# Kernel tuning notes

Measured on AMD Instinct MI355X. Metric: run time of the kernel, lower is better.

Reference implementation:

```python
import jax, jax.numpy as jnp
from jax import lax
import numpy as np

B, S, IN = 8, 4096, 64
D, H, K = 512, 8, 3
TCN_CH = [256, 256, 512]
HD = D // H


def setup_inputs() -> dict:
    key = jax.random.key(0)
    ks = iter(jax.random.split(key, 64))
    def nrm(shape, s=0.02):
        return jax.random.normal(next(ks), shape, jnp.float32) * s
    inp = {"x": jax.random.normal(next(ks), (B, S, IN), jnp.float32)}
    inp["W_in"] = nrm((IN, D)); inp["b_in"] = jnp.zeros((D,), jnp.float32)
    chans = [D] + TCN_CH
    for i in range(3):
        cin, cout = chans[i], chans[i + 1]
        inp[f"c1w{i}"] = nrm((cout, cin, K), 0.01); inp[f"c1b{i}"] = jnp.zeros((cout,), jnp.float32)
        inp[f"c2w{i}"] = nrm((cout, cout, K), 0.01); inp[f"c2b{i}"] = jnp.zeros((cout,), jnp.float32)
        if cin != cout:  # downsample 1x1 conv (blocks 0 and 2)
            inp[f"dsw{i}"] = nrm((cout, cin, 1), 0.01); inp[f"dsb{i}"] = jnp.zeros((cout,), jnp.float32)
    inp["W_tcn"] = nrm((TCN_CH[-1], D)); inp["b_tcn"] = jnp.zeros((D,), jnp.float32)
    NL = 2  # attention layers, stacked on leading axis
    for n in ["Wq", "Wk", "Wv", "Wo"]:
        inp[n] = nrm((NL, D, D))
    for n in ["bq", "bk", "bv", "bo", "ln_b"]:
        inp[n] = jnp.zeros((NL, D), jnp.float32)
    inp["ln_g"] = jnp.ones((NL, D), jnp.float32)
    inp["W_out"] = nrm((D, 1)); inp["b_out"] = jnp.zeros((1,), jnp.float32)
    return inp


def _conv(x, w, b, dil, pad):
    # x: (B,C,L), w: (O,I,K)
    y = lax.conv_general_dilated(x, w, (1,), [(pad, pad)], rhs_dilation=(dil,),
                                 dimension_numbers=("NCH", "OIH", "NCH"))
    return y + b[None, :, None]


def _block(t, c1w, c1b, c2w, c2b, ds, dil):
    # TemporalConvBlock: symmetric padding (k-1)*dil on both convs, truncate to input length
    pad = (K - 1) * dil
    o = jax.nn.relu(_conv(t, c1w, c1b, dil, pad))   # length L + pad
    o = _conv(o, c2w, c2b, dil, pad)                # length L + 2*pad
    r = t if ds is None else _conv(t, ds[0], ds[1], 1, 0)
    return jax.nn.relu(o[:, :, : t.shape[2]] + r)


def _layernorm(x, g, b, eps=1e-5):
    mu = x.mean(-1, keepdims=True)
    var = ((x - mu) ** 2).mean(-1, keepdims=True)
    return (x - mu) * lax.rsqrt(var + eps) * g + b


def _forward(x, W_in, b_in, c1w0, c1b0, c2w0, c2b0, dsw0, dsb0,
             c1w1, c1b1, c2w1, c2b1, c1w2, c1b2, c2w2, c2b2, dsw2, dsb2,
             W_tcn, b_tcn, Wq, bq, Wk, bk, Wv, bv, Wo, bo, ln_g, ln_b, W_out, b_out):
    h = x @ W_in + b_in                              # (B,S,D)
    t = jnp.swapaxes(h, 1, 2)                        # (B,D,S)
    t = _block(t, c1w0, c1b0, c2w0, c2b0, (dsw0, dsb0), 1)
    t = _block(t, c1w1, c1b1, c2w1, c2b1, None, 2)
    t = _block(t, c1w2, c1b2, c2w2, c2b2, (dsw2, dsb2), 4)
    h = h + jnp.swapaxes(t, 1, 2) @ W_tcn + b_tcn
    # sinusoidal positional encoding
    pos = jnp.arange(S, dtype=jnp.float32)[:, None]
    div = jnp.exp(jnp.arange(0, D, 2, dtype=jnp.float32) * (-np.log(10000.0) / D))
    pe = jnp.stack([jnp.sin(pos * div), jnp.cos(pos * div)], axis=-1).reshape(S, D)
    h = h + pe[None]
    for l in range(Wq.shape[0]):
        res = h
        def heads(y):  # (B,S,D) -> (B,H,S,HD)
            return y.reshape(B, S, H, HD).transpose(0, 2, 1, 3)
        q = heads(h @ Wq[l] + bq[l])
        k = heads(h @ Wk[l] + bk[l])
        v = heads(h @ Wv[l] + bv[l])
        qf = jax.nn.elu(q) + 1.0
        kf = jax.nn.elu(k) + 1.0
        kv = jnp.einsum("bhnd,bhnm->bhdm", kf, v)            # (B,H,HD,HD)
        out = jnp.einsum("bhnd,bhdm->bhnm", qf, kv)          # (B,H,S,HD)
        norm = jnp.maximum(jnp.einsum("bhnd,bhd->bhn", qf, kf.sum(2)), 1e-6)
        out = out / norm[..., None]
        out = out.transpose(0, 2, 1, 3).reshape(B, S, D)
        h = _layernorm(res + out @ Wo[l] + bo[l], ln_g[l], ln_b[l])
    pooled = h.mean(1)                                       # (B,D)
    return (pooled @ W_out + b_out)[:, 0]                    # (B,)


def reference(x, W_in, b_in, c1w0, c1b0, c2w0, c2b0, dsw0, dsb0,
              c1w1, c1b1, c2w1, c2b1, c1w2, c1b2, c2w2, c2b2, dsw2, dsb2,
              W_tcn, b_tcn, Wq, bq, Wk, bk, Wv, bv, Wo, bo, ln_g, ln_b, W_out, b_out):
    return _forward(x, W_in, b_in, c1w0, c1b0, c2w0, c2b0, dsw0, dsb0,
                    c1w1, c1b1, c2w1, c2b1, c1w2, c1b2, c2w2, c2b2, dsw2, dsb2,
                    W_tcn, b_tcn, Wq, bq, Wk, bk, Wv, bv, Wo, bo, ln_g, ln_b, W_out, b_out)
```

## Files before the change

kernel.cpp:

```cpp
#include <hip/hip_runtime.h>

typedef unsigned short u16;
typedef unsigned int u32;
typedef short bhalf8 __attribute__((ext_vector_type(8)));
typedef float f32x4 __attribute__((ext_vector_type(4)));

#define S_LEN 4096
#define NSEG 30

__device__ __forceinline__ float b2f(u16 h){ return __uint_as_float(((u32)h) << 16); }
__device__ __forceinline__ u16 f2b(float f){
  u32 u = __float_as_uint(f);
  return (u16)((u + 0x7FFFu + ((u >> 16) & 1u)) >> 16);
}
__device__ __forceinline__ u32 cvtpk(float a, float b){
  u32 r; asm("v_cvt_pk_bf16_f32 %0, %1, %2" : "=v"(r) : "v"(a), "v"(b)); return r;
}
__device__ __forceinline__ void unp8(uint4 v, float* f){
  f[0]=__uint_as_float(v.x<<16); f[1]=__uint_as_float(v.x&0xffff0000u);
  f[2]=__uint_as_float(v.y<<16); f[3]=__uint_as_float(v.y&0xffff0000u);
  f[4]=__uint_as_float(v.z<<16); f[5]=__uint_as_float(v.z&0xffff0000u);
  f[6]=__uint_as_float(v.w<<16); f[7]=__uint_as_float(v.w&0xffff0000u);
}
__device__ __forceinline__ void unp4(uint2 v, float* f){
  f[0]=__uint_as_float(v.x<<16); f[1]=__uint_as_float(v.x&0xffff0000u);
  f[2]=__uint_as_float(v.y<<16); f[3]=__uint_as_float(v.y&0xffff0000u);
}

__device__ __forceinline__ size_t taddr(int r, int c, int C){
  return (size_t)(r >> 7) * ((size_t)C << 7) + (size_t)((c >> 5) << 12)
       + ((r & 127) << 5) + (c & 31);
}

__device__ __forceinline__ void gload16(const void* g, void* l){
  __builtin_amdgcn_global_load_lds(
      (__attribute__((address_space(1))) void*)(g),
      (__attribute__((address_space(3))) void*)(l), 16, 0, 0);
}

struct PrepArgs {
  const float* src[NSEG];
  int N[NSEG]; int K[NSEG]; int sn[NSEG]; int sk[NSEG]; unsigned off[NSEG];
};

__global__ __launch_bounds__(256) void prep_w(PrepArgs pa, u16* __restrict__ wb){
  int seg = blockIdx.y;
  int N = pa.N[seg], K = pa.K[seg];
  int ntk = (K + 31) >> 5;
  int tiles = ((N + 31) >> 5) * ntk;
  int tile = blockIdx.x;
  if (tile >= tiles) return;
  int n0 = (tile / ntk) << 5, k0 = (tile % ntk) << 5;
  const float* src = pa.src[seg];
  long sn = pa.sn[seg], sk = pa.sk[seg];
  u16* dst = wb + pa.off[seg];
  int lk = threadIdx.x & 31, ln = threadIdx.x >> 5;
  #pragma unroll
  for (int i = 0; i < 4; ++i){
    int n = n0 + ln + i*8, k = k0 + lk;
    if (n < N && k < K)
      dst[(size_t)n*K + k] = f2b(src[(long)n*sn + (long)k*sk]);
  }
}

__global__ __launch_bounds__(256) void pe_k(float* __restrict__ pe){
  int id = blockIdx.x*256 + threadIdx.x;
  int s = id >> 8, i = id & 255;
  float div = expf((float)i * (-2.0f * 9.210340371976184f / 512.0f));
  float a = (float)s * div;
  pe[(size_t)s*512 + 2*i]   = sinf(a);
  pe[(size_t)s*512 + 2*i+1] = cosf(a);
}

__global__ __launch_bounds__(256) void cvt_k(const float* __restrict__ x, u16* __restrict__ xb, int n){
  int id = blockIdx.x*256 + threadIdx.x;
  if (id < n){
    int r = id >> 6, c = id & 63;
    xb[taddr(r, c, 64)] = f2b(x[id]);
  }
}

template<int NTAPS, int KS1, int KS2>
__global__ __launch_bounds__(256) void gemm_k(
    const u16* __restrict__ A, const u16* __restrict__ W,
    const u16* __restrict__ A2, const u16* __restrict__ W2,
    const float* __restrict__ bias, const float* __restrict__ bias2,
    const float* __restrict__ bias3,
    u16* __restrict__ out, const u16* __restrict__ resb,
    const float* __restrict__ peb, const float* __restrict__ den,
    int N, int CA, int CA2, int dil, int nN, int wbstride, int flags)
{
  constexpr bool MT   = (NTAPS == 3);
  constexpr int HALO  = MT ? 8 : 0;
  constexpr int AR    = MT ? 144 : 128;
  constexpr int DA    = (!MT) ? 3 : ((KS2 > 0) ? 4 : 2);
  constexpr int DB    = MT ? 4 : 3;
  constexpr int K     = KS1 << 5;
  constexpr int K2    = KS2 << 5;
  constexpr int TOTAL = MT ? (3*KS1 + KS2) : (KS1 + KS2);
  __shared__ u16 As[DA][AR*32];
  __shared__ u16 Bs[DB][128*32];
  const int tid = threadIdx.x;
  const int wave = tid >> 6, lane = tid & 63;
  const int wm = wave >> 1, wn = wave & 1;

  const int nwg = gridDim.x;
  const int lin = blockIdx.x;
  const int swz = (lin & 7) * (nwg >> 3) + (lin >> 3);
  const int mb = swz / nN, nb = swz - mb * nN;
  const int m0 = mb << 7, n0 = nb << 7;
  const bool bnd = (m0 & (S_LEN - 1)) == 0;

  const u16* Ae = (flags & 16) ? (A + (((size_t)(n0 & 511) >> 5) << 12)) : A;

  const int lr4 = lane >> 2, lc4 = lane & 3;
  const int c0 = lane >> 4, fro = lane & 15;

  const f32x4 zf = {0.f, 0.f, 0.f, 0.f};
  const bhalf8 zb = {0,0,0,0,0,0,0,0};
  f32x4 acc[4][4];
  #pragma unroll
  for (int i=0;i<4;++i)
    #pragma unroll
    for (int j=0;j<4;++j) acc[i][j] = zf;

  const u16* Wb = W + (size_t)(m0 >> 12) * (size_t)wbstride;
  const size_t abase  = (size_t)mb * ((size_t)CA  << 7);
  const size_t abase2 = (size_t)mb * ((size_t)CA2 << 7);

  auto STAGE_A = [&](int kb, int ab){
    const size_t tb = abase + ((size_t)kb << 12);
    #pragma unroll
    for (int half = 0; half < 2; ++half){
      int mrow = (wave << 5) + (half << 4) + lr4;
      int i = mrow + HALO;
      int cg = lc4 ^ ((i >> 1) & 3);
      gload16(Ae + tb + mrow*32 + (cg << 3), &As[ab][(HALO + (wave << 5) + (half << 4)) * 32]);
    }
    if (MT && wave == 0 && lane < 32){
      int j = lr4;
      int cg = lc4 ^ ((j >> 1) & 3);
      size_t hb_ = (mb ? abase - ((size_t)CA << 7) : abase) + ((size_t)kb << 12) + (120 + j)*32;
      gload16(Ae + hb_ + (cg << 3), &As[ab][0]);
    }
  };
  auto STAGE_A2 = [&](int t2, int ab){
    const size_t tb = abase2 + ((size_t)t2 << 12);
    #pragma unroll
    for (int half = 0; half < 2; ++half){
      int mrow = (wave << 5) + (half << 4) + lr4;
      int i = mrow + HALO;
      int cg = lc4 ^ ((i >> 1) & 3);
      gload16(A2 + tb + mrow*32 + (cg << 3), &As[ab][(HALO + (wave << 5) + (half << 4)) * 32]);
    }
  };
  auto STAGE_B = [&](const u16* Wt, size_t kstride, int kb, int bb){
    #pragma unroll
    for (int half = 0; half < 2; ++half){
      int i = (wave << 5) + (half << 4) + lr4;
      int cg = lc4 ^ ((i >> 1) & 3);
      gload16(Wt + (size_t)(n0 + i) * kstride + (kb << 5) + (cg << 3),
              &Bs[bb][((wave << 5) + (half << 4)) * 32]);
    }
  };
  auto DO16 = [&](int ab, int bb, int sh, bool mask){
    bhalf8 af[4], bf[4];
    #pragma unroll
    for (int mt = 0; mt < 4; ++mt){
      int r8 = (wm << 6) + (mt << 4) + fro + HALO + sh;
      af[mt] = *(const bhalf8*)&As[ab][r8 * 32 + ((c0 ^ ((r8 >> 1) & 3)) << 3)];
    }
    if (MT && mask && bnd && wm == 0 && fro + sh < 0) af[0] = zb;
    #pragma unroll
    for (int nt = 0; nt < 4; ++nt){
      int rB = (wn << 6) + (nt << 4) + fro;
      bf[nt] = *(const bhalf8*)&Bs[bb][rB * 32 + ((c0 ^ ((rB >> 1) & 3)) << 3)];
    }
    #pragma unroll
    for (int mt = 0; mt < 4; ++mt)
      #pragma unroll
      for (int nt = 0; nt < 4; ++nt)
        acc[mt][nt] = __builtin_amdgcn_mfma_f32_16x16x32_bf16(bf[nt], af[mt], acc[mt][nt], 0, 0, 0);
  };

  if constexpr (!MT){
    auto STG = [&](int s){
      int b = s % 3;
      if (s < KS1){ STAGE_A(s, b); STAGE_B(Wb, (size_t)K, s, b); }
      else if (KS2 > 0){ STAGE_A2(s - KS1, b); STAGE_B(W2, (size_t)K2, s - KS1, b); }
    };
    STG(0);
    if constexpr (TOTAL > 1) STG(1);
    #pragma unroll
    for (int s = 0; s < TOTAL; ++s){
      if (s + 1 >= TOTAL) asm volatile("s_waitcnt vmcnt(0)" ::: "memory");
      else                asm volatile("s_waitcnt vmcnt(4)" ::: "memory");
      __builtin_amdgcn_sched_barrier(0);
      __builtin_amdgcn_s_barrier();
      __builtin_amdgcn_sched_barrier(0);
      if (s + 2 < TOTAL) STG(s + 2);
      DO16(s % 3, s % 3, 0, false);
    }
  } else {
    auto STG = [&](int s){
      if (s < 3*KS1){
        int kb = s / 3, tap = s % 3;
        if (tap == 0) STAGE_A(kb, kb & (DA-1));
        STAGE_B(Wb + (size_t)tap * N * K, (size_t)K, kb, s & 3);
      } else if (KS2 > 0){
        int t2 = s - 3*KS1;
        STAGE_A2(t2, (KS1 + t2) & (DA-1));
        STAGE_B(W2, (size_t)K2, t2, s & 3);
      }
    };
    STG(0);
    if constexpr (TOTAL > 1) STG(1);
    if constexpr (TOTAL > 2) STG(2);
    #pragma unroll
    for (int s = 0; s < TOTAL; ++s){
      if (s + 1 >= TOTAL)      asm volatile("s_waitcnt vmcnt(0)" ::: "memory");
      else if (s + 2 >= TOTAL) asm volatile("s_waitcnt vmcnt(2)" ::: "memory");
      else                     asm volatile("s_waitcnt vmcnt(4)" ::: "memory");
      __builtin_amdgcn_sched_barrier(0);
      __builtin_amdgcn_s_barrier();
      __builtin_amdgcn_sched_barrier(0);
      if (s + 3 < TOTAL) STG(s + 3);
      if (s < 3*KS1) DO16((s/3) & (DA-1), s & 3, ((s%3) - 2) * dil, true);
      else           DO16((KS1 + (s - 3*KS1)) & (DA-1), s & 3, 0, false);
    }
  }

  const int mb_l = (wm << 6) + fro;
  const int cb_l = (wn << 6) + (c0 << 2);
  const int th = n0 >> 9;
  #pragma unroll
  for (int mt = 0; mt < 4; ++mt){
    const int row = m0 + mb_l + (mt << 4);
    const size_t prow = (size_t)(row & (S_LEN - 1)) * 512;
    #pragma unroll
    for (int nt = 0; nt < 4; ++nt){
      const int col = n0 + cb_l + (nt << 4);
      float v0 = acc[mt][nt][0], v1 = acc[mt][nt][1], v2 = acc[mt][nt][2], v3 = acc[mt][nt][3];
      if (flags & 32){
        const float* bp = (th == 0) ? bias : ((th == 1) ? bias2 : bias3);
        if (bp){ float4 b4 = *(const float4*)&bp[col & 511]; v0+=b4.x; v1+=b4.y; v2+=b4.z; v3+=b4.w; }
      } else {
        if (bias) { float4 b4 = *(const float4*)&bias[col];  v0+=b4.x; v1+=b4.y; v2+=b4.z; v3+=b4.w; }
        if (bias2){ float4 b4 = *(const float4*)&bias2[col]; v0+=b4.x; v1+=b4.y; v2+=b4.z; v3+=b4.w; }
      }
      if (flags & 4){
        uint2 rv = *(const uint2*)(resb + taddr(row, col, N));
        float rf[4]; unp4(rv, rf);
        v0 += rf[0]; v1 += rf[1]; v2 += rf[2]; v3 += rf[3];
      }
      if (flags & 8){
        float4 p4 = *(const float4*)&peb[prow + col];
        v0 += p4.x; v1 += p4.y; v2 += p4.z; v3 += p4.w;
      }
      if (flags & 16){
        float d = fmaxf(den[((size_t)row << 3) + (col >> 6)], 1e-6f);
        float rd = 1.0f / d;
        v0 *= rd; v1 *= rd; v2 *= rd; v3 *= rd;
      }
      if (flags & 1){
        v0 = fmaxf(v0, 0.f); v1 = fmaxf(v1, 0.f); v2 = fmaxf(v2, 0.f); v3 = fmaxf(v3, 0.f);
      }
      if ((flags & 2) && (!(flags & 32) || th < 2)){
        v0 = (v0 > 0.f) ? (v0 + 1.f) : __expf(v0);
        v1 = (v1 > 0.f) ? (v1 + 1.f) : __expf(v1);
        v2 = (v2 > 0.f) ? (v2 + 1.f) : __expf(v2);
        v3 = (v3 > 0.f) ? (v3 + 1.f) : __expf(v3);
      }
      uint2 pk; pk.x = cvtpk(v0, v1); pk.y = cvtpk(v2, v3);
      *(uint2*)(out + taddr(row, col, N)) = pk;
    }
  }
}

__global__ __launch_bounds__(256) void kv_partial(
    const u16* __restrict__ qkv,
    float* __restrict__ kvp, float* __restrict__ ksp)
{
  const int bh = blockIdx.x;
  const int b = bh >> 3, h = bh & 7;
  const int ch = blockIdx.y;
  const int t = threadIdx.x;
  __shared__ u16 kfs[16][64];
  __shared__ u16 vs[16][64];
  float acc[4][4] = {{0.f}};
  float ks[4] = {0.f,0.f,0.f,0.f};
  const int d0 = (t >> 4) << 2;
  const int c0 = (t & 15) << 2;
  const int lr = t >> 4, lc = (t & 15) << 2;
  const int rowbase = (b << 12) + (ch << 9);
  const int ck = 512 + (h << 6) + lc;
  const int cv = 1024 + (h << 6) + lc;
  for (int g = 0; g < 32; ++g){
    int r = rowbase + (g << 4) + lr;
    *(uint2*)&kfs[lr][lc] = *(const uint2*)(qkv + taddr(r, ck, 1536));
    *(uint2*)&vs[lr][lc]  = *(const uint2*)(qkv + taddr(r, cv, 1536));
    __syncthreads();
    #pragma unroll
    for (int i = 0; i < 16; ++i){
      float kv4[4], vv4[4];
      unp4(*(const uint2*)&kfs[i][d0], kv4);
      unp4(*(const uint2*)&vs[i][c0], vv4);
      #pragma unroll
      for (int j=0;j<4;++j)
        #pragma unroll
        for (int k2=0;k2<4;++k2) acc[j][k2] += kv4[j]*vv4[k2];
      if ((t & 15) == 0){
        #pragma unroll
        for (int j=0;j<4;++j) ks[j] += kv4[j];
      }
    }
    __syncthreads();
  }
  float* dst = kvp + ((size_t)(bh << 3) + ch) * 4096;
  #pragma unroll
  for (int j=0;j<4;++j)
    #pragma unroll
    for (int k2=0;k2<4;++k2) dst[(d0+j)*64 + (c0+k2)] = acc[j][k2];
  if ((t & 15) == 0){
    float* kd = ksp + ((size_t)(bh << 3) + ch) * 64;
    #pragma unroll
    for (int j=0;j<4;++j) kd[d0+j] = ks[j];
  }
}

__global__ __launch_bounds__(256) void kvred_k(
    const float* __restrict__ kvp, const float* __restrict__ ksp,
    float* __restrict__ kvf, float* __restrict__ ksf)
{
  int bh = blockIdx.x, t = threadIdx.x;
  for (int e = t; e < 4096; e += 256){
    float s = 0.f;
    #pragma unroll
    for (int ch = 0; ch < 8; ++ch) s += kvp[((size_t)(bh<<3)+ch)*4096 + e];
    kvf[(size_t)bh*4096 + e] = s;
  }
  if (t < 64){
    float s = 0.f;
    #pragma unroll
    for (int ch = 0; ch < 8; ++ch) s += ksp[((size_t)(bh<<3)+ch)*64 + t];
    ksf[bh*64 + t] = s;
  }
}

__global__ __launch_bounds__(256) void den_k(const u16* __restrict__ qkv,
    const float* __restrict__ ksf, float* __restrict__ den)
{
  int id = blockIdx.x*256 + threadIdx.x;
  int r = id >> 3, h = id & 7;
  int b = r >> 12;
  const float* ks = ksf + ((b<<3)+h)*64;
  float s = 0.f;
  for (int d = 0; d < 64; d += 8){
    uint4 vq = *(const uint4*)(qkv + taddr(r, (h << 6) + d, 1536));
    float f[8]; unp8(vq, f);
    #pragma unroll
    for (int j=0;j<8;++j) s += f[j]*ks[d+j];
  }
  den[id] = s;
}

__global__ __launch_bounds__(256) void packkv2_k(const float* __restrict__ kvf, u16* __restrict__ wbd){
  int id = blockIdx.x*256 + threadIdx.x;
  int b = id >> 16;
  int n = (id >> 7) & 511, j = id & 127;
  float v = 0.f;
  if ((j >> 6) == ((n >> 6) & 1))
    v = kvf[((size_t)((b<<3)+(n>>6)))*4096 + (j & 63)*64 + (n & 63)];
  wbd[id] = f2b(v);
}

__global__ __launch_bounds__(256) void ln_k(const u16* __restrict__ in,
    const float* __restrict__ g, const float* __restrict__ beta, u16* __restrict__ out)
{
  int wave = threadIdx.x >> 6, lane = threadIdx.x & 63;
  int row = blockIdx.x*4 + wave;
  size_t ad = taddr(row, lane*8, 512);
  uint4 pv = *(const uint4*)(in + ad);
  float f[8]; unp8(pv, f);
  float s = 0.f, ss = 0.f;
  #pragma unroll
  for (int i=0;i<8;++i){ s += f[i]; ss += f[i]*f[i]; }
  for (int m=1;m<64;m<<=1){ s += __shfl_xor(s,m); ss += __shfl_xor(ss,m); }
  float mean = s * (1.f/512.f);
  float var = ss * (1.f/512.f) - mean*mean;
  float rstd = rsqrtf(fmaxf(var, 0.f) + 1e-5f);
  u16 o[8];
  #pragma unroll
  for (int i=0;i<8;++i){
    int c = lane*8 + i;
    o[i] = f2b((f[i]-mean)*rstd*g[c] + beta[c]);
  }
  *(uint4*)(out + ad) = *(uint4*)o;
}

__global__ __launch_bounds__(256) void pool1_k(const u16* __restrict__ hb,
    const float* __restrict__ wout, const float* __restrict__ g,
    const float* __restrict__ beta, float* __restrict__ part)
{
  int b = blockIdx.x >> 6, ch = blockIdx.x & 63;
  int t = threadIdx.x;
  __shared__ float ws[512];
  __shared__ float red[256];
  __shared__ float S2[2];
  float a0 = 0.f, a1 = 0.f;
  for (int i = t; i < 512; i += 256){
    float w = wout[i];
    float gw = w * g[i];
    ws[i] = gw;
    a0 += gw;
    a1 += w * beta[i];
  }
  red[t] = a0; __syncthreads();
  for (int k2=128;k2;k2>>=1){ if (t<k2) red[t]+=red[t+k2]; __syncthreads(); }
  if (!t) S2[0] = red[0];
  __syncthreads();
  red[t] = a1; __syncthreads();
  for (int k2=128;k2;k2>>=1){ if (t<k2) red[t]+=red[t+k2]; __syncthreads(); }
  if (!t) S2[1] = red[0];
  __syncthreads();
  const float Sgw = S2[0], Sbw = S2[1];

  int r = (b << 12) + (ch << 6) + (t >> 2);
  int c0 = (t & 3) << 7;
  float sd = 0.f, s1 = 0.f, s2 = 0.f;
  for (int i = 0; i < 128; i += 8){
    uint4 v = *(const uint4*)(hb + taddr(r, c0 + i, 512));
    float f[8]; unp8(v, f);
    #pragma unroll
    for (int j=0;j<8;++j){ float x = f[j]; sd += x*ws[c0+i+j]; s1 += x; s2 += x*x; }
  }
  sd += __shfl_xor(sd,1); s1 += __shfl_xor(s1,1); s2 += __shfl_xor(s2,1);
  sd += __shfl_xor(sd,2); s1 += __shfl_xor(s1,2); s2 += __shfl_xor(s2,2);
  float mean = s1 * (1.f/512.f);
  float var  = s2 * (1.f/512.f) - mean*mean;
  float rstd = rsqrtf(fmaxf(var, 0.f) + 1e-5f);
  float rowv = rstd * (sd - mean * Sgw) + Sbw;
  red[t] = ((t & 3) == 0) ? rowv : 0.f;
  __syncthreads();
  for (int k2=128;k2;k2>>=1){ if (t<k2) red[t]+=red[t+k2]; __syncthreads(); }
  if (!t) part[blockIdx.x] = red[0];
}

__global__ __launch_bounds__(64) void pool2_k(const float* __restrict__ part,
    const float* __restrict__ bout, float* __restrict__ out)
{
  int b = blockIdx.x, t = threadIdx.x;
  float s = part[(b << 6) + t];
  for (int m=1;m<64;m<<=1) s += __shfl_xor(s,m);
  if (!t) out[b] = s * (1.f/4096.f) + bout[0];
}

extern "C" void kernel_launch(void* const* d_in, const int* in_sizes, int n_in,
                              void* d_out, int out_size, void* d_ws, size_t ws_size,
                              hipStream_t stream)
{
  (void)in_sizes; (void)n_in; (void)out_size; (void)ws_size;
  const float* x    = (const float*)d_in[0];
  const float* W_in = (const float*)d_in[1];
  const float* b_in = (const float*)d_in[2];
  const float* c1w0 = (const float*)d_in[3];
  const float* c1b0 = (const float*)d_in[4];
  const float* c2w0 = (const float*)d_in[5];
  const float* c2b0 = (const float*)d_in[6];
  const float* dsw0 = (const float*)d_in[7];
  const float* dsb0 = (const float*)d_in[8];
  const float* c1w1 = (const float*)d_in[9];
  const float* c1b1 = (const float*)d_in[10];
  const float* c2w1 = (const float*)d_in[11];
  const float* c2b1 = (const float*)d_in[12];
  const float* c1w2 = (const float*)d_in[13];
  const float* c1b2 = (const float*)d_in[14];
  const float* c2w2 = (const float*)d_in[15];
  const float* c2b2 = (const float*)d_in[16];
  const float* dsw2 = (const float*)d_in[17];
  const float* dsb2 = (const float*)d_in[18];
  const float* W_tcn= (const float*)d_in[19];
  const float* b_tcn= (const float*)d_in[20];
  const float* Wq   = (const float*)d_in[21];
  const float* Wk   = (const float*)d_in[22];
  const float* Wv   = (const float*)d_in[23];
  const float* Wo   = (const float*)d_in[24];
  const float* bq   = (const float*)d_in[25];
  const float* bk   = (const float*)d_in[26];
  const float* bv   = (const float*)d_in[27];
  const float* bo   = (const float*)d_in[28];
  const float* lnb  = (const float*)d_in[29];
  const float* lng  = (const float*)d_in[30];
  const float* W_out= (const float*)d_in[31];
  const float* b_out= (const float*)d_in[32];

  char* base = (char*)d_ws;
  size_t off = 0;
  auto alloc = [&](size_t bytes) -> void* {
    void* p = base + off;
    off += (bytes + 255) & ~(size_t)255;
    return p;
  };
  u16* WB   = (u16*)alloc(4816896ull*2);
  u16* wbd  = (u16*)alloc(8ull*512*128*2);
  float* peb= (float*)alloc(4096ull*512*4);
  float* den= (float*)alloc(32768ull*8*4);
  float* kvp= (float*)alloc(512ull*4096*4);
  float* ksp= (float*)alloc(512ull*64*4);
  float* kvf= (float*)alloc(64ull*4096*4);
  float* ksf= (float*)alloc(64ull*64*4);
  float* part=(float*)alloc(512*4);
  u16* hb   = (u16*)alloc(32768ull*512*2);
  char* qkvR= (char*)alloc(32768ull*1536*2);
  u16* atto = (u16*)alloc(32768ull*512*2);

  u16* qkvb = (u16*)qkvR;
  u16* xb   = (u16*)(qkvR);
  u16* t1b  = (u16*)(qkvR + 4194304);
  u16* t2b  = (u16*)(qkvR + 20971520);
  u16* t3b  = (u16*)(qkvR + 37748736);
  u16* o1b  = atto;

  unsigned wo_ = 0;
  auto wseg = [&](unsigned e){ unsigned o = wo_; wo_ += e; return o; };
  unsigned oWin  = wseg(512*64);
  unsigned oC1w0 = wseg(3*256*512);
  unsigned oC2w0 = wseg(3*256*256);
  unsigned oDs0  = wseg(256*512);
  unsigned oC1w1 = wseg(3*256*256);
  unsigned oC2w1 = wseg(3*256*256);
  unsigned oC1w2 = wseg(3*512*256);
  unsigned oC2w2 = wseg(3*512*512);
  unsigned oDs2  = wseg(512*256);
  unsigned oWtcn = wseg(512*512);
  unsigned oQKV  = wseg(2*1536*512);
  unsigned oWo   = wseg(2*512*512);

  PrepArgs pa;
  int si = 0;
  auto seg = [&](const float* s, int N, int K, int sn, int sk, unsigned o){
    pa.src[si]=s; pa.N[si]=N; pa.K[si]=K; pa.sn[si]=sn; pa.sk[si]=sk; pa.off[si]=o; ++si;
  };
  seg(W_in, 512, 64, 1, 512, oWin);
  for (int t=0;t<3;++t) seg(c1w0 + t, 256, 512, 1536, 3, oC1w0 + t*131072);
  for (int t=0;t<3;++t) seg(c2w0 + t, 256, 256,  768, 3, oC2w0 + t*65536);
  seg(dsw0, 256, 512, 512, 1, oDs0);
  for (int t=0;t<3;++t) seg(c1w1 + t, 256, 256,  768, 3, oC1w1 + t*65536);
  for (int t=0;t<3;++t) seg(c2w1 + t, 256, 256,  768, 3, oC2w1 + t*65536);
  for (int t=0;t<3;++t) seg(c1w2 + t, 512, 256,  768, 3, oC1w2 + t*131072);
  for (int t=0;t<3;++t) seg(c2w2 + t, 512, 512, 1536, 3, oC2w2 + t*262144);
  seg(dsw2, 512, 256, 256, 1, oDs2);
  seg(W_tcn, 512, 512, 1, 512, oWtcn);
  for (int l=0;l<2;++l){
    seg(Wq + l*262144, 512, 512, 1, 512, oQKV + l*786432 + 0);
    seg(Wk + l*262144, 512, 512, 1, 512, oQKV + l*786432 + 262144);
    seg(Wv + l*262144, 512, 512, 1, 512, oQKV + l*786432 + 524288);
  }
  for (int l=0;l<2;++l) seg(Wo + l*262144, 512, 512, 1, 512, oWo + l*262144);

  prep_w<<<dim3(256, NSEG), 256, 0, stream>>>(pa, WB);
  pe_k<<<4096, 256, 0, stream>>>(peb);
  cvt_k<<<8192, 256, 0, stream>>>(x, xb, 32768*64);

  const int RELU=1, ELU1=2, RES=4, PE=8, DIV=16, QKV=32;
  auto gemm = [&](const u16* A, const u16* W, const u16* A2, const u16* W2,
                  const float* b1, const float* b2, const float* b3,
                  u16* out, const u16* resb,
                  int K, int K2, int N, int CA, int CA2, int ntaps,
                  int dil, int wbs, int flags){
    int nN = N >> 7;
    dim3 grid(256 * nN);
    if (ntaps == 3){
      if (K == 512 && K2 == 0)
        gemm_k<3,16,0><<<grid, 256, 0, stream>>>(A, W, A2, W2, b1, b2, b3, out, resb,
                                                 peb, den, N, CA, CA2, dil, nN, wbs, flags);
      else if (K == 256 && K2 == 512)
        gemm_k<3,8,16><<<grid, 256, 0, stream>>>(A, W, A2, W2, b1, b2, b3, out, resb,
                                                 peb, den, N, CA, CA2, dil, nN, wbs, flags);
      else if (K == 256 && K2 == 0)
        gemm_k<3,8,0><<<grid, 256, 0, stream>>>(A, W, A2, W2, b1, b2, b3, out, resb,
                                                peb, den, N, CA, CA2, dil, nN, wbs, flags);
      else
        gemm_k<3,16,8><<<grid, 256, 0, stream>>>(A, W, A2, W2, b1, b2, b3, out, resb,
                                                 peb, den, N, CA, CA2, dil, nN, wbs, flags);
    } else {
      if (K == 64)
        gemm_k<1,2,0><<<grid, 256, 0, stream>>>(A, W, A2, W2, b1, b2, b3, out, resb,
                                                peb, den, N, CA, CA2, dil, nN, wbs, flags);
      else if (K == 128)
        gemm_k<1,4,0><<<grid, 256, 0, stream>>>(A, W, A2, W2, b1, b2, b3, out, resb,
                                                peb, den, N, CA, CA2, dil, nN, wbs, flags);
      else
        gemm_k<1,16,0><<<grid, 256, 0, stream>>>(A, W, A2, W2, b1, b2, b3, out, resb,
                                                 peb, den, N, CA, CA2, dil, nN, wbs, flags);
    }
  };

  gemm(xb, WB + oWin, nullptr, nullptr, b_in, nullptr, nullptr, hb, nullptr,
       64, 0, 512, 64, 0, 1, 1, 0, 0);
  gemm(hb,  WB + oC1w0, nullptr, nullptr, c1b0, nullptr, nullptr, o1b, nullptr,
       512, 0, 256, 512, 0, 3, 1, 0, RELU);
  gemm(o1b, WB + oC2w0, hb, WB + oDs0, c2b0, dsb0, nullptr, t1b, nullptr,
       256, 512, 256, 256, 512, 3, 1, 0, RELU);
  gemm(t1b, WB + oC1w1, nullptr, nullptr, c1b1, nullptr, nullptr, o1b, nullptr,
       256, 0, 256, 256, 0, 3, 2, 0, RELU);
  gemm(o1b, WB + oC2w1, nullptr, nullptr, c2b1, nullptr, nullptr, t2b, t1b,
       256, 0, 256, 256, 0, 3, 2, 0, RELU|RES);
  gemm(t2b, WB + oC1w2, nullptr, nullptr, c1b2, nullptr, nullptr, o1b, nullptr,
       256, 0, 512, 256, 0, 3, 4, 0, RELU);
  gemm(o1b, WB + oC2w2, t2b, WB + oDs2, c2b2, dsb2, nullptr, t3b, nullptr,
       512, 256, 512, 512, 256, 3, 4, 0, RELU);
  gemm(t3b, WB + oWtcn, nullptr, nullptr, b_tcn, nullptr, nullptr, hb, hb,
       512, 0, 512, 512, 0, 1, 1, 0, RES|PE);

  for (int l = 0; l < 2; ++l){
    gemm(hb, WB + oQKV + l*786432, nullptr, nullptr, bq + l*512, bk + l*512, bv + l*512,
         qkvb, nullptr, 512, 0, 1536, 512, 0, 1, 1, 0, ELU1|QKV);
    kv_partial<<<dim3(64, 8), 256, 0, stream>>>(qkvb, kvp, ksp);
    kvred_k<<<64, 256, 0, stream>>>(kvp, ksp, kvf, ksf);
    den_k<<<1024, 256, 0, stream>>>(qkvb, ksf, den);
    packkv2_k<<<2048, 256, 0, stream>>>(kvf, wbd);
    gemm(qkvb, wbd, nullptr, nullptr, nullptr, nullptr, nullptr, atto, nullptr,
         128, 0, 512, 1536, 0, 1, 1, 512*128, DIV);
    gemm(atto, WB + oWo + l*262144, nullptr, nullptr, bo + l*512, nullptr, nullptr, hb, hb,
         512, 0, 512, 512, 0, 1, 1, 0, RES);
    if (l == 0)
      ln_k<<<8192, 256, 0, stream>>>(hb, lng, lnb, hb);
  }

  pool1_k<<<512, 256, 0, stream>>>(hb, W_out, lng + 512, lnb + 512, part);
  pool2_k<<<8, 64, 0, stream>>>(part, b_out, (float*)d_out);
}
```

Before: 781.9 us.

## Add 256x256-tile 8-wave pipelined GEMM kernel for K=512 dense projections

Adds a new GEMM kernel with 256x256 output tiles, 512 threads and double-buffered, XOR-swizzled LDS staging. The main loop interleaves global loads, LDS fragment reads and MFMA work in quarter-steps, with explicit barriers and priority hints. It replaces the 1x1 projection GEMMs with K=512 (TCN output, QKV, Wo), aiming at more operand reuse per tile and better latency hiding. In exchange it uses one workgroup per CU with a large LDS footprint, and the removed K=512 branch of the old kernel now falls through to the K=128 template, which could be wrong if anything still takes that path.

```diff
diff --git a/kernel.cpp b/kernel.cpp
--- a/kernel.cpp
+++ b/kernel.cpp
@@ -77,6 +77,172 @@
   if (id < n){
     int r = id >> 6, c = id & 63;
     xb[taddr(r, c, 64)] = f2b(x[id]);
+  }
+}
+
+template<int KTOT>
+__global__ __launch_bounds__(512, 1) void gemm8_k(
+    const u16* __restrict__ A, const u16* __restrict__ W,
+    const float* __restrict__ bias, const float* __restrict__ bias2,
+    const float* __restrict__ bias3,
+    u16* __restrict__ out, const u16* __restrict__ resb,
+    const float* __restrict__ peb,
+    int N, int nN, int flags)
+{
+  constexpr int KT = KTOT >> 6;
+  constexpr int IT = KT >> 1;
+  __shared__ u16 As[2][16384];
+  __shared__ u16 Bs[2][16384];
+  const int tid = threadIdx.x;
+  const int wave = tid >> 6, lane = tid & 63;
+  const int wm = wave >> 2, wn = wave & 3;
+  const int c0 = lane >> 4, fro = lane & 15;
+
+  const int nwg = gridDim.x;
+  const int lin = blockIdx.x;
+  const int swz = (lin & 7) * (nwg >> 3) + (lin >> 3);
+  const int mb = swz / nN, nb = swz - mb * nN;
+  const int m0 = mb << 8, n0 = nb << 8;
+
+  const f32x4 zf = {0.f,0.f,0.f,0.f};
+  f32x4 acc[8][4];
+  #pragma unroll
+  for (int i=0;i<8;++i)
+    #pragma unroll
+    for (int j=0;j<4;++j) acc[i][j] = zf;
+
+  bhalf8 af[2][2], bf[4][2];
+
+  auto SA = [&](int t, int q){
+    int s = (q << 9) + tid;
+    int row = s >> 3, phys = s & 7;
+    int lc = phys ^ (row & 7);
+    int grow = m0 + row;
+    int gcol = (t << 6) + (lc << 3);
+    size_t ga = ((size_t)(grow >> 7) << 16) + (size_t)((gcol >> 5) << 12)
+              + ((grow & 127) << 5) + (gcol & 31);
+    gload16(A + ga, &As[t & 1][(q << 12) + (wave << 9)]);
+  };
+  auto SB = [&](int t, int j){
+    int s = (j << 9) + tid;
+    int row = s >> 3, phys = s & 7;
+    int lc = phys ^ (row & 7);
+    gload16(W + (size_t)(n0 + row) * KTOT + (t << 6) + (lc << 3),
+            &Bs[t & 1][(j << 12) + (wave << 9)]);
+  };
+  auto LDB = [&](int t){
+    #pragma unroll
+    for (int nt=0;nt<4;++nt)
+      #pragma unroll
+      for (int ks=0;ks<2;++ks){
+        int row = (wn << 6) + (nt << 4) + fro;
+        int phys = ((ks << 2) + c0) ^ (row & 7);
+        bf[nt][ks] = *(const bhalf8*)&Bs[t & 1][(row << 6) + (phys << 3)];
+      }
+  };
+  auto LDA = [&](int t, int q){
+    #pragma unroll
+    for (int mtl=0;mtl<2;++mtl)
+      #pragma unroll
+      for (int ks=0;ks<2;++ks){
+        int row = (q << 6) + (wm << 5) + (mtl << 4) + fro;
+        int phys = ((ks << 2) + c0) ^ (row & 7);
+        af[mtl][ks] = *(const bhalf8*)&As[t & 1][(row << 6) + (phys << 3)];
+      }
+  };
+  auto BAR = [&]{
+    __builtin_amdgcn_sched_barrier(0);
+    __builtin_amdgcn_s_barrier();
+    __builtin_amdgcn_sched_barrier(0);
+  };
+  auto MM = [&](int q){
+    __builtin_amdgcn_s_setprio(1);
+    #pragma unroll
+    for (int mtl=0;mtl<2;++mtl)
+      #pragma unroll
+      for (int nt=0;nt<4;++nt){
+        acc[(q<<1)+mtl][nt] = __builtin_amdgcn_mfma_f32_16x16x32_bf16(
+            bf[nt][0], af[mtl][0], acc[(q<<1)+mtl][nt], 0, 0, 0);
+        acc[(q<<1)+mtl][nt] = __builtin_amdgcn_mfma_f32_16x16x32_bf16(
+            bf[nt][1], af[mtl][1], acc[(q<<1)+mtl][nt], 0, 0, 0);
+      }
+    __builtin_amdgcn_s_setprio(0);
+  };
+
+  #pragma unroll
+  for (int x=0;x<4;++x){ SA(0,x); SB(0,x); }
+  #pragma unroll
+  for (int x=0;x<3;++x){ SA(1,x); SB(1,x); }
+  asm volatile("s_waitcnt vmcnt(6)" ::: "memory");
+  BAR();
+
+  #pragma unroll
+  for (int i=0;i<IT;++i){
+    const int t0 = 2*i, t1 = 2*i+1, t2 = 2*i+2, t3 = 2*i+3;
+    #pragma unroll
+    for (int q=0;q<4;++q){
+      if (q == 0) LDB(t0);
+      LDA(t0, q);
+      if (q == 0){ SA(t1,3); SB(t1,3); }
+      else if (t2 < KT){ SA(t2,q-1); SB(t2,q-1); }
+      BAR();
+      MM(q);
+      if (q == 3){
+        if (t2 < KT) asm volatile("s_waitcnt vmcnt(6)" ::: "memory");
+        else         asm volatile("s_waitcnt vmcnt(0)" ::: "memory");
+      }
+      BAR();
+    }
+    #pragma unroll
+    for (int q=0;q<4;++q){
+      if (q == 0) LDB(t1);
+      LDA(t1, q);
+      if (q == 0){ if (t2 < KT){ SA(t2,3); SB(t2,3); } }
+      else if (t3 < KT){ SA(t3,q-1); SB(t3,q-1); }
+      BAR();
+      MM(q);
+      if (q == 3 && (i + 1 < IT))
+        asm volatile("s_waitcnt vmcnt(6)" ::: "memory");
+      BAR();
+    }
+  }
+
+  const int th = n0 >> 9;
+  #pragma unroll
+  for (int mt = 0; mt < 8; ++mt){
+    const int row = m0 + ((mt >> 1) << 6) + (wm << 5) + ((mt & 1) << 4) + fro;
+    const size_t prow = (size_t)(row & (S_LEN - 1)) * 512;
+    #pragma unroll
+    for (int nt = 0; nt < 4; ++nt){
+      const int col = n0 + (wn << 6) + (nt << 4) + (c0 << 2);
+      float v0 = acc[mt][nt][0], v1 = acc[mt][nt][1], v2 = acc[mt][nt][2], v3 = acc[mt][nt][3];
+      if (flags & 32){
+        const float* bp = (th == 0) ? bias : ((th == 1) ? bias2 : bias3);
+        if (bp){ float4 b4 = *(const float4*)&bp[col & 511]; v0+=b4.x; v1+=b4.y; v2+=b4.z; v3+=b4.w; }
+      } else {
+        if (bias){ float4 b4 = *(const float4*)&bias[col]; v0+=b4.x; v1+=b4.y; v2+=b4.z; v3+=b4.w; }
+      }
+      if (flags & 4){
+        uint2 rv = *(const uint2*)(resb + taddr(row, col, N));
+        float rf[4]; unp4(rv, rf);
+        v0 += rf[0]; v1 += rf[1]; v2 += rf[2]; v3 += rf[3];
+      }
+      if (flags & 8){
+        float4 p4 = *(const float4*)&peb[prow + col];
+        v0 += p4.x; v1 += p4.y; v2 += p4.z; v3 += p4.w;
+      }
+      if (flags & 1){
+        v0 = fmaxf(v0, 0.f); v1 = fmaxf(v1, 0.f); v2 = fmaxf(v2, 0.f); v3 = fmaxf(v3, 0.f);
+      }
+      if ((flags & 2) && (!(flags & 32) || th < 2)){
+        v0 = (v0 > 0.f) ? (v0 + 1.f) : __expf(v0);
+        v1 = (v1 > 0.f) ? (v1 + 1.f) : __expf(v1);
+        v2 = (v2 > 0.f) ? (v2 + 1.f) : __expf(v2);
+        v3 = (v3 > 0.f) ? (v3 + 1.f) : __expf(v3);
+      }
+      uint2 pk; pk.x = cvtpk(v0, v1); pk.y = cvtpk(v2, v3);
+      *(uint2*)(out + taddr(row, col, N)) = pk;
+    }
   }
 }
 
@@ -587,13 +753,16 @@
       if (K == 64)
         gemm_k<1,2,0><<<grid, 256, 0, stream>>>(A, W, A2, W2, b1, b2, b3, out, resb,
                                                 peb, den, N, CA, CA2, dil, nN, wbs, flags);
-      else if (K == 128)
+      else
         gemm_k<1,4,0><<<grid, 256, 0, stream>>>(A, W, A2, W2, b1, b2, b3, out, resb,
                                                 peb, den, N, CA, CA2, dil, nN, wbs, flags);
-      else
-        gemm_k<1,16,0><<<grid, 256, 0, stream>>>(A, W, A2, W2, b1, b2, b3, out, resb,
-                                                 peb, den, N, CA, CA2, dil, nN, wbs, flags);
-    }
+    }
+  };
+  auto gemm8 = [&](const u16* A, const u16* W, const float* b1, const float* b2,
+                   const float* b3, u16* out, const u16* resb, int N, int flags){
+    int nN = N >> 8;
+    gemm8_k<512><<<dim3(128 * nN), 512, 0, stream>>>(A, W, b1, b2, b3, out, resb,
+                                                     peb, N, nN, flags);
   };
 
   gemm(xb, WB + oWin, nullptr, nullptr, b_in, nullptr, nullptr, hb, nullptr,
@@ -610,20 +779,18 @@
        256, 0, 512, 256, 0, 3, 4, 0, RELU);
   gemm(o1b, WB + oC2w2, t2b, WB + oDs2, c2b2, dsb2, nullptr, t3b, nullptr,
        512, 256, 512, 512, 256, 3, 4, 0, RELU);
-  gemm(t3b, WB + oWtcn, nullptr, nullptr, b_tcn, nullptr, nullptr, hb, hb,
-       512, 0, 512, 512, 0, 1, 1, 0, RES|PE);
+  gemm8(t3b, WB + oWtcn, b_tcn, nullptr, nullptr, hb, hb, 512, RES|PE);
 
   for (int l = 0; l < 2; ++l){
-    gemm(hb, WB + oQKV + l*786432, nullptr, nullptr, bq + l*512, bk + l*512, bv + l*512,
-         qkvb, nullptr, 512, 0, 1536, 512, 0, 1, 1, 0, ELU1|QKV);
+    gemm8(hb, WB + oQKV + l*786432, bq + l*512, bk + l*512, bv + l*512,
+          qkvb, nullptr, 1536, ELU1|QKV);
     kv_partial<<<dim3(64, 8), 256, 0, stream>>>(qkvb, kvp, ksp);
     kvred_k<<<64, 256, 0, stream>>>(kvp, ksp, kvf, ksf);
     den_k<<<1024, 256, 0, stream>>>(qkvb, ksf, den);
     packkv2_k<<<2048, 256, 0, stream>>>(kvf, wbd);
     gemm(qkvb, wbd, nullptr, nullptr, nullptr, nullptr, nullptr, atto, nullptr,
          128, 0, 512, 1536, 0, 1, 1, 512*128, DIV);
-    gemm(atto, WB + oWo + l*262144, nullptr, nullptr, bo + l*512, nullptr, nullptr, hb, hb,
-         512, 0, 512, 512, 0, 1, 1, 0, RES);
+    gemm8(atto, WB + oWo + l*262144, bo + l*512, nullptr, nullptr, hb, hb, 512, RES);
     if (l == 0)
       ln_k<<<8192, 256, 0, stream>>>(hb, lng, lnb, hb);
   }
```

Result: no change. 774.7 us (-0.9%).
